# Optimization experiments

Hardware: AMD Instinct MI355X
Metric: run time of the kernel (lower is better)

Reference implementation:

```python
import jax, jax.numpy as jnp
import numpy as np

B, C, T = 4, 1024, 2048
H = 16            # num_heads
G = 32            # GroupNorm groups (normalization(channels) == GroupNorm(32, C))
EPS = 1e-5


def setup_inputs() -> dict:
    key = jax.random.key(0)
    ks = jax.random.split(key, 7)
    x = jax.random.normal(ks[0], (B, C, T), dtype=jnp.float32)
    gn_scale = jax.random.normal(ks[1], (C,), dtype=jnp.float32) * 0.02 + 1.0
    gn_bias = jax.random.normal(ks[2], (C,), dtype=jnp.float32) * 0.02
    qkv_w = jax.random.normal(ks[3], (3 * C, C), dtype=jnp.float32) / np.sqrt(C)
    qkv_b = jax.random.normal(ks[4], (3 * C,), dtype=jnp.float32) * 0.02
    # NOTE: original zero-inits proj_out; randomized here so output != x for testing.
    proj_w = jax.random.normal(ks[5], (C, C), dtype=jnp.float32) / np.sqrt(C)
    proj_b = jax.random.normal(ks[6], (C,), dtype=jnp.float32) * 0.02
    return {"x": x, "gn_scale": gn_scale, "gn_bias": gn_bias,
            "qkv_w": qkv_w, "qkv_b": qkv_b, "proj_w": proj_w, "proj_b": proj_b}


def reference(x, gn_scale, gn_bias, qkv_w, qkv_b, proj_w, proj_b):
    b, c, t = x.shape
    ch = c // H
    # GroupNorm(32, C) over (channels-in-group, T)
    xg = x.reshape(b, G, c // G, t)
    mean = xg.mean(axis=(2, 3), keepdims=True)
    var = xg.var(axis=(2, 3), keepdims=True)
    xn = ((xg - mean) * jax.lax.rsqrt(var + EPS)).reshape(b, c, t)
    xn = xn * gn_scale[None, :, None] + gn_bias[None, :, None]
    # 1x1 conv QKV: [B, 3C, T]
    qkv = jnp.einsum('oc,bct->bot', qkv_w, xn) + qkv_b[None, :, None]
    q, k, v = jnp.split(qkv, 3, axis=1)
    # split heads -> [B*H, ch, T]
    q = q.reshape(b * H, ch, t)
    k = k.reshape(b * H, ch, t)
    v = v.reshape(b * H, ch, t)
    scale = 1.0 / np.sqrt(np.sqrt(ch)).astype(np.float32)
    # full T x T attention weights, softmax in fp32 (as original)
    w = jnp.einsum('bct,bcs->bts', q * scale, k * scale)
    w = jax.nn.softmax(w.astype(jnp.float32), axis=-1).astype(w.dtype)
    a = jnp.einsum('bts,bcs->bct', w, v).reshape(b, c, t)
    # 1x1 conv projection + residual
    h = jnp.einsum('oc,bct->bot', proj_w, a) + proj_b[None, :, None]
    return x + h
```

## Files before the change

### kernel.cpp

```cpp
#include <hip/hip_runtime.h>
#include <hip/hip_bf16.h>
#include <stdint.h>

#define Bn 4
#define Cn 1024
#define Tn 2048
#define Hn 16
#define Gn 32
#define SCALE_Q 0.18033688f

typedef short short8  __attribute__((ext_vector_type(8)));
typedef short short4_t __attribute__((ext_vector_type(4)));
typedef float float4_t __attribute__((ext_vector_type(4)));

__device__ __forceinline__ short f2bf(float f) {
    uint32_t u = __float_as_uint(f);
    uint32_t r = (u + 0x7FFFu + ((u >> 16) & 1u)) >> 16;
    return (short)r;
}

__device__ __forceinline__ float exp2_fast(float x) {
#if __has_builtin(__builtin_amdgcn_exp2f)
    return __builtin_amdgcn_exp2f(x);
#else
    return exp2f(x);
#endif
}

__device__ __forceinline__ uint32_t pack_bf16_trunc(float lo, float hi) {
#if __has_builtin(__builtin_amdgcn_perm)
    return __builtin_amdgcn_perm(__float_as_uint(hi), __float_as_uint(lo), 0x07060302u);
#else
    return (__float_as_uint(lo) >> 16) | (__float_as_uint(hi) & 0xFFFF0000u);
#endif
}

__device__ __forceinline__ float4_t mfma16(short4_t a, short4_t b, float4_t c) {
#if __has_builtin(__builtin_amdgcn_mfma_f32_16x16x16bf16_1k)
    return __builtin_amdgcn_mfma_f32_16x16x16bf16_1k(a, b, c, 0, 0, 0);
#else
    short8 az = {a[0], a[1], a[2], a[3], 0, 0, 0, 0};
    short8 bz = {b[0], b[1], b[2], b[3], 0, 0, 0, 0};
    return __builtin_amdgcn_mfma_f32_16x16x32_bf16(az, bz, c, 0, 0, 0);
#endif
}

#define GLL16(gptr, lptr)                                                      \
    __builtin_amdgcn_global_load_lds(                                          \
        (const __attribute__((address_space(1))) unsigned int*)(gptr),         \
        (__attribute__((address_space(3))) unsigned int*)(lptr), 16, 0, 0)

__global__ __launch_bounds__(256) void cvt_w(const float* __restrict__ src,
                                             short* __restrict__ dst, int n4) {
    int i = blockIdx.x * 256 + threadIdx.x;
    if (i < n4) {
        float4_t v = reinterpret_cast<const float4_t*>(src)[i];
        short4_t o;
        o[0] = f2bf(v[0]); o[1] = f2bf(v[1]); o[2] = f2bf(v[2]); o[3] = f2bf(v[3]);
        reinterpret_cast<short4_t*>(dst)[i] = o;
    }
}

__global__ __launch_bounds__(256) void groupnorm_k(const float* __restrict__ x,
                                                   const float* __restrict__ gs,
                                                   const float* __restrict__ gb,
                                                   short* __restrict__ xnT) {
    int blk = blockIdx.x;
    int b = blk >> 5, g = blk & 31;
    const float* base = x + ((size_t)(b * Cn + g * 32)) * Tn;
    int tid = threadIdx.x;

    float s = 0.f, ss = 0.f;
    const float4_t* b4 = reinterpret_cast<const float4_t*>(base);
    for (int i = tid; i < 16384; i += 256) {
        float4_t v = b4[i];
        s  += v[0] + v[1] + v[2] + v[3];
        ss += v[0]*v[0] + v[1]*v[1] + v[2]*v[2] + v[3]*v[3];
    }
    #pragma unroll
    for (int m = 1; m < 64; m <<= 1) { s += __shfl_xor(s, m); ss += __shfl_xor(ss, m); }
    __shared__ float red[8];
    int wave = tid >> 6;
    if ((tid & 63) == 0) { red[wave * 2] = s; red[wave * 2 + 1] = ss; }
    __syncthreads();
    float ts  = red[0] + red[2] + red[4] + red[6];
    float tss = red[1] + red[3] + red[5] + red[7];
    float mean = ts * (1.f / 65536.f);
    float var  = tss * (1.f / 65536.f) - mean * mean;
    float rstd = rsqrtf(var + 1e-5f);

    __shared__ float tile[64][33];
    for (int t0 = 0; t0 < Tn; t0 += 64) {
        #pragma unroll
        for (int k = 0; k < 8; k++) {
            int e = tid + k * 256;
            int c = e >> 6, tt = e & 63;
            float v = base[c * Tn + t0 + tt];
            tile[tt][c] = (v - mean) * rstd * gs[g * 32 + c] + gb[g * 32 + c];
        }
        __syncthreads();
        #pragma unroll
        for (int k = 0; k < 8; k++) {
            int f = tid + k * 256;
            int tt = f >> 5, c = f & 31;
            xnT[((size_t)(b * Tn + t0 + tt)) * Cn + g * 32 + c] = f2bf(tile[tt][c]);
        }
        __syncthreads();
    }
}

template <int MODE>
__global__ __launch_bounds__(256) void gemm_k(const short* __restrict__ W,
                                              const short* __restrict__ Bm,
                                              const float* __restrict__ bias,
                                              const float* __restrict__ xres,
                                              short* __restrict__ qkT,
                                              short* __restrict__ vbuf,
                                              float* __restrict__ outp) {
    constexpr int K = 1024;
    __shared__ short As[128 * 64];
    __shared__ short Bs[128 * 64];
    int m0 = blockIdx.x * 128, n0 = blockIdx.y * 128, b = blockIdx.z;
    int tid = threadIdx.x;
    int wave = tid >> 6, lane = tid & 63, quad = lane >> 4, l15 = lane & 15;
    int wm = wave >> 1, wn = wave & 1;
    const short* Ab = W + (size_t)m0 * K;
    const short* Bb = Bm + ((size_t)b * Tn + n0) * K;

    float4_t acc[4][4];
    float4_t z = {0.f, 0.f, 0.f, 0.f};
    #pragma unroll
    for (int i = 0; i < 4; i++)
        #pragma unroll
        for (int j = 0; j < 4; j++) acc[i][j] = z;

    int sw = l15 & 7;

    for (int k0 = 0; k0 < K; k0 += 64) {
        #pragma unroll
        for (int r = 0; r < 4; r++) {
            int cid = r * 256 + tid;
            int row = cid >> 3, j = cid & 7;
            int chunk = j ^ (row & 7);
            GLL16(Ab + (size_t)row * K + k0 + chunk * 8, As + cid * 8);
            GLL16(Bb + (size_t)row * K + k0 + chunk * 8, Bs + cid * 8);
        }
        __syncthreads();
        #pragma unroll
        for (int kk = 0; kk < 2; kk++) {
            short8 af[4], bfg[4];
            #pragma unroll
            for (int mi = 0; mi < 4; mi++)
                af[mi] = *reinterpret_cast<const short8*>(
                    &As[(wm * 64 + mi * 16 + l15) * 64 + ((4 * kk + quad) ^ sw) * 8]);
            #pragma unroll
            for (int ni = 0; ni < 4; ni++)
                bfg[ni] = *reinterpret_cast<const short8*>(
                    &Bs[(wn * 64 + ni * 16 + l15) * 64 + ((4 * kk + quad) ^ sw) * 8]);
            #pragma unroll
            for (int mi = 0; mi < 4; mi++)
                #pragma unroll
                for (int ni = 0; ni < 4; ni++)
                    acc[mi][ni] = __builtin_amdgcn_mfma_f32_16x16x32_bf16(
                        af[mi], bfg[ni], acc[mi][ni], 0, 0, 0);
        }
        __syncthreads();
    }

    if (MODE == 0) {
        #pragma unroll
        for (int mi = 0; mi < 4; mi++) {
            int mrow = m0 + wm * 64 + mi * 16 + quad * 4;
            #pragma unroll
            for (int ni = 0; ni < 4; ni++) {
                int t = n0 + wn * 64 + ni * 16 + l15;
                if (mrow < 2048) {
                    int hh = mrow >> 6, ch = mrow & 63;
                    float sc = (mrow < 1024) ? SCALE_Q : 1.0f;
                    short4_t pk;
                    #pragma unroll
                    for (int r = 0; r < 4; r++)
                        pk[r] = f2bf((acc[mi][ni][r] + bias[mrow + r]) * sc);
                    *reinterpret_cast<short4_t*>(
                        &qkT[(((size_t)b * 32 + hh) * Tn + t) * 64 + ch]) = pk;
                } else {
                    int c = mrow - 2048;
                    #pragma unroll
                    for (int r = 0; r < 4; r++)
                        vbuf[((size_t)b * Cn + c + r) * Tn + t] =
                            f2bf(acc[mi][ni][r] + bias[mrow + r]);
                }
            }
        }
    } else {
        #pragma unroll
        for (int mi = 0; mi < 4; mi++) {
            int mrow = m0 + wm * 64 + mi * 16 + quad * 4;
            #pragma unroll
            for (int ni = 0; ni < 4; ni++) {
                int t = n0 + wn * 64 + ni * 16 + l15;
                #pragma unroll
                for (int r = 0; r < 4; r++) {
                    size_t idx = ((size_t)b * Cn + mrow + r) * Tn + t;
                    outp[idx] = xres[idx] + bias[mrow + r] + acc[mi][ni][r];
                }
            }
        }
    }
}

__global__ __launch_bounds__(256, 2) void attn_k(const short* __restrict__ qkT,
                                                 const short* __restrict__ vbuf,
                                                 short* __restrict__ aT) {
    __shared__ short ks[64 * 72];
    __shared__ short vs[64 * 72];
    int bh = blockIdx.y; int b = bh >> 4, h = bh & 15;
    int t0 = blockIdx.x * 256;
    int tid = threadIdx.x;
    int wave = tid >> 6, lane = tid & 63, quad = lane >> 4, l15 = lane & 15;
    const short* qb = qkT + (((size_t)b * 32 + h) * Tn) * 64;
    const short* kb = qkT + (((size_t)b * 32 + 16 + h) * Tn) * 64;
    const short* vb = vbuf + ((size_t)b * Cn + h * 64) * Tn;
    int tw = t0 + wave * 64;

    short8 qf[4][2];
    #pragma unroll
    for (int tni = 0; tni < 4; tni++)
        #pragma unroll
        for (int kk = 0; kk < 2; kk++)
            qf[tni][kk] = *reinterpret_cast<const short8*>(
                qb + ((size_t)(tw + tni * 16 + l15)) * 64 + kk * 32 + quad * 8);

    float4_t z = {0.f, 0.f, 0.f, 0.f};
    float4_t acc[4][4];
    float lsum[4];
    #pragma unroll
    for (int i = 0; i < 4; i++) {
        lsum[i] = 0.f;
        #pragma unroll
        for (int j = 0; j < 4; j++) acc[i][j] = z;
    }

    for (int s0 = 0; s0 < Tn; s0 += 64) {
        #pragma unroll
        for (int r = 0; r < 2; r++) {
            int cid = r * 256 + tid;
            int row = cid >> 3, off = cid & 7;
            *reinterpret_cast<uint4*>(&ks[row * 72 + off * 8]) =
                *reinterpret_cast<const uint4*>(kb + ((size_t)(s0 + row)) * 64 + off * 8);
            *reinterpret_cast<uint4*>(&vs[row * 72 + off * 8]) =
                *reinterpret_cast<const uint4*>(vb + (size_t)row * Tn + s0 + off * 8);
        }
        __syncthreads();

        #pragma unroll
        for (int smi = 0; smi < 4; smi++) {
            float4_t sa[4];
            #pragma unroll
            for (int tni = 0; tni < 4; tni++) sa[tni] = z;
            #pragma unroll
            for (int kk = 0; kk < 2; kk++) {
                short8 kf = *reinterpret_cast<const short8*>(
                    &ks[(smi * 16 + l15) * 72 + kk * 32 + quad * 8]);
                #pragma unroll
                for (int tni = 0; tni < 4; tni++)
                    sa[tni] = __builtin_amdgcn_mfma_f32_16x16x32_bf16(
                        kf, qf[tni][kk], sa[tni], 0, 0, 0);
            }
            short4_t vf[4];
            #pragma unroll
            for (int ci = 0; ci < 4; ci++)
                vf[ci] = *reinterpret_cast<const short4_t*>(
                    &vs[(ci * 16 + l15) * 72 + smi * 16 + quad * 4]);
            #pragma unroll
            for (int tni = 0; tni < 4; tni++) {
                float p0 = exp2_fast(sa[tni][0]);
                float p1 = exp2_fast(sa[tni][1]);
                float p2 = exp2_fast(sa[tni][2]);
                float p3 = exp2_fast(sa[tni][3]);
                uint32_t u0 = __float_as_uint(p0), u1 = __float_as_uint(p1);
                uint32_t u2 = __float_as_uint(p2), u3 = __float_as_uint(p3);
                lsum[tni] += __uint_as_float(u0 & 0xFFFF0000u)
                           + __uint_as_float(u1 & 0xFFFF0000u)
                           + __uint_as_float(u2 & 0xFFFF0000u)
                           + __uint_as_float(u3 & 0xFFFF0000u);
                uint2 pk;
                pk.x = pack_bf16_trunc(p0, p1);
                pk.y = pack_bf16_trunc(p2, p3);
                short4_t pf = *reinterpret_cast<short4_t*>(&pk);
                #pragma unroll
                for (int ci = 0; ci < 4; ci++)
                    acc[tni][ci] = mfma16(pf, vf[ci], acc[tni][ci]);
            }
        }
        __syncthreads();
    }

    #pragma unroll
    for (int tni = 0; tni < 4; tni++) {
        lsum[tni] += __shfl_xor(lsum[tni], 16);
        lsum[tni] += __shfl_xor(lsum[tni], 32);
    }

    #pragma unroll
    for (int tmi = 0; tmi < 4; tmi++) {
        float rl[4];
        #pragma unroll
        for (int r = 0; r < 4; r++)
            rl[r] = 1.0f / __shfl(lsum[tmi], quad * 4 + r);
        #pragma unroll
        for (int ci = 0; ci < 4; ci++)
            #pragma unroll
            for (int r = 0; r < 4; r++) {
                int t = tw + tmi * 16 + quad * 4 + r;
                int ch = ci * 16 + l15;
                aT[((size_t)b * Tn + t) * Cn + h * 64 + ch] =
                    f2bf(acc[tmi][ci][r] * rl[r]);
            }
    }
}

extern "C" void kernel_launch(void* const* d_in, const int* in_sizes, int n_in,
                              void* d_out, int out_size, void* d_ws, size_t ws_size,
                              hipStream_t stream) {
    const float* x     = (const float*)d_in[0];
    const float* gs    = (const float*)d_in[1];
    const float* gb    = (const float*)d_in[2];
    const float* qkvw  = (const float*)d_in[3];
    const float* qkvb  = (const float*)d_in[4];
    const float* projw = (const float*)d_in[5];
    const float* projb = (const float*)d_in[6];
    float* out = (float*)d_out;

    char* ws = (char*)d_ws;
    short* wqkv  = (short*)(ws + 0);
    short* wproj = (short*)(ws + 6291456);
    short* xnT   = (short*)(ws + 8388608);
    short* aT    = (short*)(ws + 8388608);
    short* qkT   = (short*)(ws + 25165824);
    short* vbuf  = (short*)(ws + 58720256);

    cvt_w<<<dim3(3072), dim3(256), 0, stream>>>(qkvw, wqkv, 786432);
    cvt_w<<<dim3(1024), dim3(256), 0, stream>>>(projw, wproj, 262144);
    groupnorm_k<<<dim3(Bn * Gn), dim3(256), 0, stream>>>(x, gs, gb, xnT);
    gemm_k<0><<<dim3(24, 16, 4), dim3(256), 0, stream>>>(wqkv, xnT, qkvb, nullptr,
                                                         qkT, vbuf, nullptr);
    attn_k<<<dim3(8, 64), dim3(256), 0, stream>>>(qkT, vbuf, aT);
    gemm_k<1><<<dim3(8, 16, 4), dim3(256), 0, stream>>>(wproj, aT, projb, x,
                                                        nullptr, nullptr, out);
}
```

Measured before the change: 321.4 us.

## Use 16x16x32 MFMA for PV with permlane swaps and MFMA row sums

The attention kernel now runs 512 threads per block, with each wave owning 32 query rows instead of 64. This halves per-wave accumulator registers and raises occupancy. The P·V product uses the wider 16x16x32 bf16 MFMA: two score tiles are rearranged into the K=32 operand layout with permlane32/permlane16 swaps. The softmax denominator now comes from an MFMA against a ones vector instead of scalar adds and shuffles. This cuts VALU and shuffle work but relies on gfx950 permlane swap instructions and on the lane mapping being correct.

```diff
diff --git a/kernel.cpp b/kernel.cpp
--- a/kernel.cpp
+++ b/kernel.cpp
@@ -12,6 +12,7 @@
 typedef short short8  __attribute__((ext_vector_type(8)));
 typedef short short4_t __attribute__((ext_vector_type(4)));
 typedef float float4_t __attribute__((ext_vector_type(4)));
+typedef unsigned int uint2_t __attribute__((ext_vector_type(2)));
 
 __device__ __forceinline__ short f2bf(float f) {
     uint32_t u = __float_as_uint(f);
@@ -35,13 +36,20 @@
 #endif
 }
 
-__device__ __forceinline__ float4_t mfma16(short4_t a, short4_t b, float4_t c) {
-#if __has_builtin(__builtin_amdgcn_mfma_f32_16x16x16bf16_1k)
-    return __builtin_amdgcn_mfma_f32_16x16x16bf16_1k(a, b, c, 0, 0, 0);
+__device__ __forceinline__ void permswap32(uint32_t& x, uint32_t& y) {
+#if __has_builtin(__builtin_amdgcn_permlane32_swap)
+    uint2_t r = __builtin_amdgcn_permlane32_swap(x, y, false, false);
+    x = r[0]; y = r[1];
 #else
-    short8 az = {a[0], a[1], a[2], a[3], 0, 0, 0, 0};
-    short8 bz = {b[0], b[1], b[2], b[3], 0, 0, 0, 0};
-    return __builtin_amdgcn_mfma_f32_16x16x32_bf16(az, bz, c, 0, 0, 0);
+    asm volatile("v_permlane32_swap_b32 %0, %1" : "+v"(x), "+v"(y));
+#endif
+}
+__device__ __forceinline__ void permswap16(uint32_t& x, uint32_t& y) {
+#if __has_builtin(__builtin_amdgcn_permlane16_swap)
+    uint2_t r = __builtin_amdgcn_permlane16_swap(x, y, false, false);
+    x = r[0]; y = r[1];
+#else
+    asm volatile("v_permlane16_swap_b32 %0, %1" : "+v"(x), "+v"(y));
 #endif
 }
 
@@ -209,7 +217,7 @@
     }
 }
 
-__global__ __launch_bounds__(256, 2) void attn_k(const short* __restrict__ qkT,
+__global__ __launch_bounds__(512, 4) void attn_k(const short* __restrict__ qkT,
                                                  const short* __restrict__ vbuf,
                                                  short* __restrict__ aT) {
     __shared__ short ks[64 * 72];
@@ -221,31 +229,32 @@
     const short* qb = qkT + (((size_t)b * 32 + h) * Tn) * 64;
     const short* kb = qkT + (((size_t)b * 32 + 16 + h) * Tn) * 64;
     const short* vb = vbuf + ((size_t)b * Cn + h * 64) * Tn;
-    int tw = t0 + wave * 64;
-
-    short8 qf[4][2];
-    #pragma unroll
-    for (int tni = 0; tni < 4; tni++)
+    int tw = t0 + wave * 32;
+
+    short8 qf[2][2];
+    #pragma unroll
+    for (int tni = 0; tni < 2; tni++)
         #pragma unroll
         for (int kk = 0; kk < 2; kk++)
             qf[tni][kk] = *reinterpret_cast<const short8*>(
                 qb + ((size_t)(tw + tni * 16 + l15)) * 64 + kk * 32 + quad * 8);
 
+    short8 ones;
+    #pragma unroll
+    for (int i = 0; i < 8; i++) ones[i] = (short)0x3F80;
+
     float4_t z = {0.f, 0.f, 0.f, 0.f};
-    float4_t acc[4][4];
-    float lsum[4];
-    #pragma unroll
-    for (int i = 0; i < 4; i++) {
-        lsum[i] = 0.f;
+    float4_t acc[2][4], lacc[2];
+    #pragma unroll
+    for (int i = 0; i < 2; i++) {
+        lacc[i] = z;
         #pragma unroll
         for (int j = 0; j < 4; j++) acc[i][j] = z;
     }
 
     for (int s0 = 0; s0 < Tn; s0 += 64) {
-        #pragma unroll
-        for (int r = 0; r < 2; r++) {
-            int cid = r * 256 + tid;
-            int row = cid >> 3, off = cid & 7;
+        {
+            int row = tid >> 3, off = tid & 7;
             *reinterpret_cast<uint4*>(&ks[row * 72 + off * 8]) =
                 *reinterpret_cast<const uint4*>(kb + ((size_t)(s0 + row)) * 64 + off * 8);
             *reinterpret_cast<uint4*>(&vs[row * 72 + off * 8]) =
@@ -254,69 +263,68 @@
         __syncthreads();
 
         #pragma unroll
-        for (int smi = 0; smi < 4; smi++) {
-            float4_t sa[4];
-            #pragma unroll
-            for (int tni = 0; tni < 4; tni++) sa[tni] = z;
-            #pragma unroll
-            for (int kk = 0; kk < 2; kk++) {
-                short8 kf = *reinterpret_cast<const short8*>(
-                    &ks[(smi * 16 + l15) * 72 + kk * 32 + quad * 8]);
-                #pragma unroll
-                for (int tni = 0; tni < 4; tni++)
-                    sa[tni] = __builtin_amdgcn_mfma_f32_16x16x32_bf16(
-                        kf, qf[tni][kk], sa[tni], 0, 0, 0);
-            }
-            short4_t vf[4];
+        for (int pr = 0; pr < 2; pr++) {
+            uint32_t pk[2][2][2];
+            #pragma unroll
+            for (int half = 0; half < 2; half++) {
+                int smi = pr * 2 + half;
+                float4_t sa[2] = {z, z};
+                #pragma unroll
+                for (int kk = 0; kk < 2; kk++) {
+                    short8 kf = *reinterpret_cast<const short8*>(
+                        &ks[(smi * 16 + l15) * 72 + kk * 32 + quad * 8]);
+                    #pragma unroll
+                    for (int tni = 0; tni < 2; tni++)
+                        sa[tni] = __builtin_amdgcn_mfma_f32_16x16x32_bf16(
+                            kf, qf[tni][kk], sa[tni], 0, 0, 0);
+                }
+                #pragma unroll
+                for (int tni = 0; tni < 2; tni++) {
+                    float p0 = exp2_fast(sa[tni][0]);
+                    float p1 = exp2_fast(sa[tni][1]);
+                    float p2 = exp2_fast(sa[tni][2]);
+                    float p3 = exp2_fast(sa[tni][3]);
+                    pk[half][tni][0] = pack_bf16_trunc(p0, p1);
+                    pk[half][tni][1] = pack_bf16_trunc(p2, p3);
+                }
+            }
+            short8 vf[4];
             #pragma unroll
             for (int ci = 0; ci < 4; ci++)
-                vf[ci] = *reinterpret_cast<const short4_t*>(
-                    &vs[(ci * 16 + l15) * 72 + smi * 16 + quad * 4]);
-            #pragma unroll
-            for (int tni = 0; tni < 4; tni++) {
-                float p0 = exp2_fast(sa[tni][0]);
-                float p1 = exp2_fast(sa[tni][1]);
-                float p2 = exp2_fast(sa[tni][2]);
-                float p3 = exp2_fast(sa[tni][3]);
-                uint32_t u0 = __float_as_uint(p0), u1 = __float_as_uint(p1);
-                uint32_t u2 = __float_as_uint(p2), u3 = __float_as_uint(p3);
-                lsum[tni] += __uint_as_float(u0 & 0xFFFF0000u)
-                           + __uint_as_float(u1 & 0xFFFF0000u)
-                           + __uint_as_float(u2 & 0xFFFF0000u)
-                           + __uint_as_float(u3 & 0xFFFF0000u);
-                uint2 pk;
-                pk.x = pack_bf16_trunc(p0, p1);
-                pk.y = pack_bf16_trunc(p2, p3);
-                short4_t pf = *reinterpret_cast<short4_t*>(&pk);
+                vf[ci] = *reinterpret_cast<const short8*>(
+                    &vs[(ci * 16 + l15) * 72 + pr * 32 + quad * 8]);
+            #pragma unroll
+            for (int tni = 0; tni < 2; tni++) {
+                uint32_t x0 = pk[0][tni][0], y0 = pk[1][tni][0];
+                permswap32(x0, y0); permswap16(x0, y0);
+                uint32_t x1 = pk[0][tni][1], y1 = pk[1][tni][1];
+                permswap32(x1, y1); permswap16(x1, y1);
+                uint4 afu = {x0, x1, y0, y1};
+                short8 af = *reinterpret_cast<short8*>(&afu);
+                lacc[tni] = __builtin_amdgcn_mfma_f32_16x16x32_bf16(
+                    af, ones, lacc[tni], 0, 0, 0);
                 #pragma unroll
                 for (int ci = 0; ci < 4; ci++)
-                    acc[tni][ci] = mfma16(pf, vf[ci], acc[tni][ci]);
-            }
-        }
-        __syncthreads();
-    }
-
-    #pragma unroll
-    for (int tni = 0; tni < 4; tni++) {
-        lsum[tni] += __shfl_xor(lsum[tni], 16);
-        lsum[tni] += __shfl_xor(lsum[tni], 32);
-    }
-
-    #pragma unroll
-    for (int tmi = 0; tmi < 4; tmi++) {
-        float rl[4];
-        #pragma unroll
-        for (int r = 0; r < 4; r++)
-            rl[r] = 1.0f / __shfl(lsum[tmi], quad * 4 + r);
-        #pragma unroll
-        for (int ci = 0; ci < 4; ci++)
-            #pragma unroll
-            for (int r = 0; r < 4; r++) {
-                int t = tw + tmi * 16 + quad * 4 + r;
+                    acc[tni][ci] = __builtin_amdgcn_mfma_f32_16x16x32_bf16(
+                        af, vf[ci], acc[tni][ci], 0, 0, 0);
+            }
+        }
+        __syncthreads();
+    }
+
+    #pragma unroll
+    for (int tni = 0; tni < 2; tni++) {
+        #pragma unroll
+        for (int r = 0; r < 4; r++) {
+            float rl = 1.0f / lacc[tni][r];
+            int t = tw + tni * 16 + quad * 4 + r;
+            #pragma unroll
+            for (int ci = 0; ci < 4; ci++) {
                 int ch = ci * 16 + l15;
                 aT[((size_t)b * Tn + t) * Cn + h * 64 + ch] =
-                    f2bf(acc[tmi][ci][r] * rl[r]);
-            }
+                    f2bf(acc[tni][ci][r] * rl);
+            }
+        }
     }
 }
 
@@ -345,7 +353,7 @@
     groupnorm_k<<<dim3(Bn * Gn), dim3(256), 0, stream>>>(x, gs, gb, xnT);
     gemm_k<0><<<dim3(24, 16, 4), dim3(256), 0, stream>>>(wqkv, xnT, qkvb, nullptr,
                                                          qkT, vbuf, nullptr);
-    attn_k<<<dim3(8, 64), dim3(256), 0, stream>>>(qkT, vbuf, aT);
+    attn_k<<<dim3(8, 64), dim3(512), 0, stream>>>(qkT, vbuf, aT);
     gemm_k<1><<<dim3(8, 16, 4), dim3(256), 0, stream>>>(wproj, aT, projb, x,
                                                         nullptr, nullptr, out);
 }
```

Result: slower. 335.3 us (+4.3%).
